# Optimization experiments

Hardware: AMD Instinct MI355X
Metric: run time of the kernel (lower is better)

The kernel has to match this reference:

```python
import jax, jax.numpy as jnp
import numpy as np

N = 4096        # batch size (rows)
K = 4           # instances per class -> num_instances in the torch code
D = 256         # embedding dim
MARGIN = 0.5
SAMPLE_KEY = jax.random.key(42)  # fixed key: deterministic stand-in for torch.multinomial


def setup_inputs() -> dict:
    key = jax.random.key(0)
    x = jax.random.normal(key, (N, D), dtype=jnp.float32)
    # L2-normalize like typical metric-learning embeddings so sims are in [-1, 1]
    inputs = x / jnp.linalg.norm(x, axis=1, keepdims=True)
    targets = (jnp.arange(N) // K).astype(jnp.int32)  # P*K batch: equal-size classes
    return {"inputs": inputs, "targets": targets}


def reference(inputs, targets):
    n = inputs.shape[0]
    km1 = K - 1                 # positives per row
    n_neg = n - K               # negatives per row

    sim = inputs @ inputs.T                                   # [n, n]
    same = targets[:, None] == targets[None, :]
    eye = jnp.eye(n, dtype=bool)
    pos_mask = same & ~eye
    neg_mask = ~same

    # masked_select + per-row sort: masked entries -> +inf, ascending sort,
    # keep first count entries (counts are uniform across rows)
    pos_sorted = jnp.sort(jnp.where(pos_mask, sim, jnp.inf), axis=1)[:, :km1]   # [n, K-1]
    neg_sorted = jnp.sort(jnp.where(neg_mask, sim, jnp.inf), axis=1)[:, :n_neg] # [n, n-K]

    pos_d = jnp.mean(pos_sorted)
    neg_d = jnp.mean(neg_sorted)

    # GaussDistribution per row over negatives
    neg_mean = jnp.mean(neg_sorted, axis=1, keepdims=True)
    neg_std = jnp.sqrt(jnp.mean((neg_sorted - neg_mean) ** 2, axis=1, keepdims=True))
    # NOTE: the original uses exp(+(x-mu)^2 / (2 sigma^2)) (no minus sign) -- faithful
    logprob = (neg_sorted - neg_mean) ** 2 / (2.0 * neg_std ** 2)               # [n, n-K]

    # multinomial without replacement ~ Gumbel top-k on log-weights
    gumbel = -jnp.log(-jnp.log(
        jax.random.uniform(SAMPLE_KEY, logprob.shape, minval=1e-20, maxval=1.0)))
    _, neg_idx = jax.lax.top_k(logprob + gumbel, km1)                            # [n, K-1]
    neg_pair = jnp.take_along_axis(neg_sorted, neg_idx, axis=1)                  # [n, K-1]

    pos_loss = jnp.mean(jnp.log1p(jnp.exp(-2.0 * (pos_sorted - MARGIN))), axis=1)
    neg_loss = 0.04 * jnp.mean(jnp.log1p(jnp.exp(50.0 * (neg_pair - MARGIN))), axis=1)
    loss = jnp.sum(pos_loss + neg_loss) / n

    # prec: fraction of rows where hardest positive > hardest sampled negative + 0.05
    c = jnp.sum(pos_sorted[:, -1] > jnp.max(neg_pair, axis=1) + 0.05)
    prec = c.astype(jnp.float32) / n

    return loss, prec, pos_d, neg_d
```

## Files before the change

kernel.cpp:

```cpp
#include <hip/hip_runtime.h>
#include <hip/hip_bf16.h>
#include <cstdint>
#include <cfloat>
#include <math.h>

#define NN 4096
#define DD 256
#define NNEG 4092
#define MARGIN 0.5f
#define NB 3584
#define NW (NB / 2)
#define GTOTAL ((uint32_t)NN * (uint32_t)NNEG)

__device__ __forceinline__ uint32_t rotl32(uint32_t x, int r) {
  return (x << r) | (x >> (32 - r));
}

__device__ __forceinline__ void threefry2x32_42(uint32_t x0, uint32_t x1,
                                                uint32_t& o0, uint32_t& o1) {
  const uint32_t k0 = 0u, k1 = 42u;
  const uint32_t k2 = k0 ^ k1 ^ 0x1BD11BDAu;
  x0 += k0; x1 += k1;
#define TF_R(r) { x0 += x1; x1 = rotl32(x1, r); x1 ^= x0; }
  TF_R(13) TF_R(15) TF_R(26) TF_R(6)
  x0 += k1; x1 += k2 + 1u;
  TF_R(17) TF_R(29) TF_R(16) TF_R(24)
  x0 += k2; x1 += k0 + 2u;
  TF_R(13) TF_R(15) TF_R(26) TF_R(6)
  x0 += k0; x1 += k1 + 3u;
  TF_R(17) TF_R(29) TF_R(16) TF_R(24)
  x0 += k1; x1 += k2 + 4u;
  TF_R(13) TF_R(15) TF_R(26) TF_R(6)
  x0 += k2; x1 += k0 + 5u;
#undef TF_R
  o0 = x0; o1 = x1;
}

__device__ __forceinline__ float gumbel_at(uint32_t f) {
  uint32_t o0, o1;
  threefry2x32_42(0u, f, o0, o1);
  uint32_t bits = o0 ^ o1;
  uint32_t fb = (bits >> 9) | 0x3F800000u;
  float fl = __uint_as_float(fb) - 1.0f;
  float u = fmaxf(1e-20f, fl + 1e-20f);
  return -logf(-logf(u));
}

__device__ __forceinline__ int bucket_of(float v) {
  return (int)fminf(fmaxf((v + 0.28f) * 6400.0f, 0.0f), (float)(NB - 1));
}

#define BT 64
#define NTT (NN / BT)
#define GEMM_BLOCKS (NTT * (NTT + 1) / 2)
#define BK 64
#define LDSS 68
#define GUMBEL_BLOCKS 384

template <int GOFF>
__global__ __launch_bounds__(256) void gemm_gumbel(const float* __restrict__ X,
                                                   float* __restrict__ S,
                                                   float* __restrict__ G) {
  __shared__ float As[BT * LDSS];
  __shared__ float Bs[BT * LDSS];
  const int tid = threadIdx.x;

  if (GOFF > 0 && (int)blockIdx.x < GOFF) {
    uint32_t i = (uint32_t)blockIdx.x * 256u + (uint32_t)tid;
    const uint32_t stride = (uint32_t)GOFF * 256u;
    for (; i < GTOTAL; i += stride) G[i] = gumbel_at(i);
    return;
  }

  const int tx = tid & 15, ty = tid >> 4;

  int b = (int)blockIdx.x - GOFF, bi = 0;
  while (b >= NTT - bi) { b -= NTT - bi; bi++; }
  const int bj = bi + b;
  const int rowBase = bi * BT, colBase = bj * BT;

  float acc[4][4] = {};
  for (int kb = 0; kb < DD; kb += BK) {
#pragma unroll
    for (int it = 0; it < 4; ++it) {
      int idx = tid + 256 * it;
      int r = idx >> 4, c4 = idx & 15;
      float4 av = *(const float4*)(X + (size_t)(rowBase + r) * DD + kb + c4 * 4);
      float4 bv = *(const float4*)(X + (size_t)(colBase + r) * DD + kb + c4 * 4);
      *(float4*)(As + r * LDSS + c4 * 4) = av;
      *(float4*)(Bs + r * LDSS + c4 * 4) = bv;
    }
    __syncthreads();
    for (int k = 0; k < BK; k += 4) {
      float4 a[4], bfr[4];
#pragma unroll
      for (int i = 0; i < 4; ++i) a[i] = *(const float4*)(As + (ty + 16 * i) * LDSS + k);
#pragma unroll
      for (int j = 0; j < 4; ++j) bfr[j] = *(const float4*)(Bs + (tx + 16 * j) * LDSS + k);
#pragma unroll
      for (int i = 0; i < 4; ++i)
#pragma unroll
        for (int j = 0; j < 4; ++j) {
          acc[i][j] += a[i].x * bfr[j].x;
          acc[i][j] += a[i].y * bfr[j].y;
          acc[i][j] += a[i].z * bfr[j].z;
          acc[i][j] += a[i].w * bfr[j].w;
        }
    }
    __syncthreads();
  }
#pragma unroll
  for (int i = 0; i < 4; ++i)
#pragma unroll
    for (int j = 0; j < 4; ++j)
      S[(size_t)(rowBase + ty + 16 * i) * NN + colBase + tx + 16 * j] = acc[i][j];
  if (bi != bj) {
#pragma unroll
    for (int i = 0; i < 4; ++i)
#pragma unroll
      for (int j = 0; j < 4; ++j)
        S[(size_t)(colBase + tx + 16 * j) * NN + rowBase + ty + 16 * i] = acc[i][j];
  }
}

#define INSERT3(sc, v)                                              \
  if ((sc) > s2) {                                                  \
    if ((sc) > s1) {                                                \
      s2 = s1; v2 = v1;                                             \
      if ((sc) > s0) { s1 = s0; v1 = v0; s0 = (sc); v0 = (v); }     \
      else           { s1 = (sc); v1 = (v); }                       \
    } else { s2 = (sc); v2 = (v); }                                 \
  }

template <int USE_G>
__global__ __launch_bounds__(256) void row_kernel(const float* __restrict__ S,
                                                  const float* __restrict__ G,
                                                  float* __restrict__ acc) {
  __shared__ uint32_t histw[NW];
  __shared__ uint32_t offsw[NW];
  __shared__ __align__(16) float sval[NN];
  __shared__ float sh[48];
  __shared__ uint32_t wtot[4];

  const int row = blockIdx.x;
  const int tid = threadIdx.x;
  const int lane = tid & 63, wid = tid >> 6;

#pragma unroll
  for (int i = 0; i < 7; ++i) histw[tid + 256 * i] = 0u;

  const float4* src = (const float4*)(S + (size_t)row * NN);
  const int pslot = row >> 2;
  float vv[16];
#pragma unroll
  for (int it = 0; it < 4; ++it) {
    int slot = tid + 256 * it;
    float4 t4 = src[slot];
    if (slot == pslot) {
      sh[16] = t4.x; sh[17] = t4.y; sh[18] = t4.z; sh[19] = t4.w;
      t4.x = INFINITY; t4.y = INFINITY; t4.z = INFINITY; t4.w = INFINITY;
    }
    vv[4 * it + 0] = t4.x; vv[4 * it + 1] = t4.y;
    vv[4 * it + 2] = t4.z; vv[4 * it + 3] = t4.w;
  }

  float s = 0.0f;
#pragma unroll
  for (int e = 0; e < 16; ++e) if (vv[e] < 1e30f) s += vv[e];
#pragma unroll
  for (int off = 32; off > 0; off >>= 1) s += __shfl_down(s, off, 64);
  if (lane == 0) sh[5 + wid] = s;
  __syncthreads();

#pragma unroll
  for (int e = 0; e < 16; ++e) {
    int b = bucket_of(vv[e]);
    atomicAdd(&histw[b >> 1], 1u << ((b & 1) << 4));
  }
  if (tid == 0) {
    int self = row & 3;
    float p[3]; int m = 0;
#pragma unroll
    for (int c = 0; c < 4; ++c)
      if (c != self) p[m++] = sh[16 + c];
    float t;
    if (p[0] > p[1]) { t = p[0]; p[0] = p[1]; p[1] = t; }
    if (p[1] > p[2]) { t = p[1]; p[1] = p[2]; p[2] = t; }
    if (p[0] > p[1]) { t = p[0]; p[0] = p[1]; p[1] = t; }
    sh[0] = p[0]; sh[1] = p[1]; sh[2] = p[2];
    float tot = sh[5] + sh[6] + sh[7] + sh[8];
    sh[9] = tot;
    sh[3] = tot / (float)NNEG;
  }
  __syncthreads();

  uint32_t hw[7];
  uint32_t s14 = 0;
#pragma unroll
  for (int j = 0; j < 7; ++j) {
    hw[j] = histw[7 * tid + j];
    s14 += (hw[j] & 0xFFFFu) + (hw[j] >> 16);
  }
  uint32_t inc = s14;
#pragma unroll
  for (int off = 1; off < 64; off <<= 1) {
    uint32_t n = __shfl_up(inc, (unsigned)off, 64);
    if (lane >= off) inc += n;
  }
  if (lane == 63) wtot[wid] = inc;

  const float mu = sh[3];
  float q = 0.0f;
#pragma unroll
  for (int e = 0; e < 16; ++e)
    if (vv[e] < 1e30f) { float d = vv[e] - mu; q += d * d; }
#pragma unroll
  for (int off = 32; off > 0; off >>= 1) q += __shfl_down(q, off, 64);
  if (lane == 0) sh[10 + wid] = q;
  __syncthreads();

  uint32_t wbase = 0;
  for (int w = 0; w < wid; ++w) wbase += wtot[w];
  uint32_t run = wbase + inc - s14;
#pragma unroll
  for (int j = 0; j < 7; ++j) {
    uint32_t lo = run; run += hw[j] & 0xFFFFu;
    uint32_t hi = run; run += hw[j] >> 16;
    offsw[7 * tid + j] = lo | (hi << 16);
  }
  if (tid == 0) {
    float var = (sh[10] + sh[11] + sh[12] + sh[13]) / (float)NNEG;
    float sd = sqrtf(var);
    sh[4] = 1.0f / (2.0f * sd * sd);
  }
  __syncthreads();

#pragma unroll
  for (int e = 0; e < 16; ++e) {
    int b = bucket_of(vv[e]);
    uint32_t old = atomicAdd(&offsw[b >> 1], 1u << ((b & 1) << 4));
    uint32_t sl = (old >> ((b & 1) << 4)) & 0xFFFFu;
    sval[sl] = vv[e];
  }
  __syncthreads();

  const float inv2s2 = sh[4];
  const uint32_t fbase = (uint32_t)row * (uint32_t)NNEG;
  const float* __restrict__ Grow = G + fbase;
  float s0 = -FLT_MAX, s1 = -FLT_MAX, s2 = -FLT_MAX;
  float v0 = 0.0f, v1 = 0.0f, v2 = 0.0f;

  float va[16]; uint32_t sten[16];
#pragma unroll
  for (int it = 0; it < 16; ++it) va[it] = sval[tid + 256 * it];
#pragma unroll
  for (int it = 0; it < 16; ++it) {
    float v = va[it];
    uint32_t pk = 0u;
    if (v < 1e30f) {
      int b = bucket_of(v);
      uint32_t sh16 = (uint32_t)((b & 1) << 4);
      uint32_t end = (offsw[b >> 1] >> sh16) & 0xFFFFu;
      uint32_t cb = (histw[b >> 1] >> sh16) & 0xFFFFu;
      pk = (end - cb) | (end << 16);
    }
    sten[it] = pk;
  }

#pragma unroll
  for (int half = 0; half < 2; ++half) {
    float4 w0[8];
#pragma unroll
    for (int j = 0; j < 8; ++j) {
      uint32_t st = sten[half * 8 + j] & 0xFFFFu;
      w0[j] = *(const float4*)(sval + (st & ~3u));
    }
#pragma unroll
    for (int j = 0; j < 8; ++j) {
      const int it = half * 8 + j;
      float v = va[it];
      if (v < 1e30f) {
        const int sl = tid + 256 * it;
        const uint32_t st = sten[it] & 0xFFFFu, en = sten[it] >> 16;
        const uint32_t nb = en - st;
        const uint32_t u0 = st & ~3u;
        int cnt = (int)st;
        {
          float4 w = w0[j];
          cnt += ((u0 + 0 - st) < nb && (w.x < v || (w.x == v && (int)(u0 + 0) < sl))) ? 1 : 0;
          cnt += ((u0 + 1 - st) < nb && (w.y < v || (w.y == v && (int)(u0 + 1) < sl))) ? 1 : 0;
          cnt += ((u0 + 2 - st) < nb && (w.z < v || (w.z == v && (int)(u0 + 2) < sl))) ? 1 : 0;
          cnt += ((u0 + 3 - st) < nb && (w.w < v || (w.w == v && (int)(u0 + 3) < sl))) ? 1 : 0;
        }
        for (uint32_t u = u0 + 4; u < en; u += 4) {
          float4 w = *(const float4*)(sval + u);
          cnt += ((u + 0 - st) < nb && (w.x < v || (w.x == v && (int)(u + 0) < sl))) ? 1 : 0;
          cnt += ((u + 1 - st) < nb && (w.y < v || (w.y == v && (int)(u + 1) < sl))) ? 1 : 0;
          cnt += ((u + 2 - st) < nb && (w.z < v || (w.z == v && (int)(u + 2) < sl))) ? 1 : 0;
          cnt += ((u + 3 - st) < nb && (w.w < v || (w.w == v && (int)(u + 3) < sl))) ? 1 : 0;
        }
        float g = USE_G ? Grow[cnt] : gumbel_at(fbase + (uint32_t)cnt);
        float d = v - mu;
        float sc = d * d * inv2s2 + g;
        INSERT3(sc, v)
      }
    }
  }

#pragma unroll
  for (int dlt = 1; dlt < 64; dlt <<= 1) {
    float t0 = __shfl_xor(s0, dlt, 64), u0 = __shfl_xor(v0, dlt, 64);
    float t1 = __shfl_xor(s1, dlt, 64), u1 = __shfl_xor(v1, dlt, 64);
    float t2 = __shfl_xor(s2, dlt, 64), u2 = __shfl_xor(v2, dlt, 64);
    INSERT3(t0, u0)
    INSERT3(t1, u1)
    INSERT3(t2, u2)
  }
  if (lane == 0) {
    int b0 = 24 + wid * 6;
    sh[b0 + 0] = s0; sh[b0 + 1] = v0;
    sh[b0 + 2] = s1; sh[b0 + 3] = v1;
    sh[b0 + 4] = s2; sh[b0 + 5] = v2;
  }
  __syncthreads();

  if (tid == 0) {
    float g0 = -FLT_MAX, g1 = -FLT_MAX, g2 = -FLT_MAX;
    float w0 = 0.0f, w1 = 0.0f, w2 = 0.0f;
    {
      float s0 = g0, s1 = g1, s2 = g2, v0 = w0, v1 = w1, v2 = w2;
#pragma unroll
      for (int i = 0; i < 12; ++i) {
        float sc = sh[24 + 2 * i], v = sh[24 + 2 * i + 1];
        INSERT3(sc, v)
      }
      g0 = s0; g1 = s1; g2 = s2; w0 = v0; w1 = v1; w2 = v2;
    }
    float negmax = fmaxf(w0, fmaxf(w1, w2));
    float neg_loss = 0.04f * (log1pf(expf(50.0f * (w0 - MARGIN))) +
                              log1pf(expf(50.0f * (w1 - MARGIN))) +
                              log1pf(expf(50.0f * (w2 - MARGIN)))) / 3.0f;
    float p0 = sh[0], p1 = sh[1], p2 = sh[2];
    float pos_loss = (log1pf(expf(-2.0f * (p0 - MARGIN))) +
                      log1pf(expf(-2.0f * (p1 - MARGIN))) +
                      log1pf(expf(-2.0f * (p2 - MARGIN)))) / 3.0f;
    atomicAdd(&acc[0], pos_loss + neg_loss);
    if (p2 > negmax + 0.05f) atomicAdd(&acc[1], 1.0f);
    atomicAdd(&acc[2], p0 + p1 + p2);
    atomicAdd(&acc[3], sh[9]);
  }
}

__global__ void finalize(const float* __restrict__ acc, float* out) {
  if (threadIdx.x == 0 && blockIdx.x == 0) {
    out[0] = acc[0] / 4096.0f;
    out[1] = acc[1] / 4096.0f;
    out[2] = acc[2] / (4096.0f * 3.0f);
    out[3] = acc[3] / (4096.0f * 4092.0f);
  }
}

extern "C" void kernel_launch(void* const* d_in, const int* in_sizes, int n_in,
                              void* d_out, int out_size, void* d_ws, size_t ws_size,
                              hipStream_t stream) {
  (void)in_sizes; (void)n_in; (void)out_size;
  const float* X = (const float*)d_in[0];
  float* S = (float*)d_ws;
  float* acc = (float*)((char*)d_ws + (size_t)NN * NN * 4);
  float* G = (float*)((char*)d_ws + (size_t)NN * NN * 4 + 256);
  const size_t need = (size_t)NN * NN * 4 + 256 + (size_t)GTOTAL * 4;
  const bool have_g = ws_size >= need;

  hipMemsetAsync(acc, 0, 4 * sizeof(float), stream);
  if (have_g) {
    gemm_gumbel<GUMBEL_BLOCKS><<<GUMBEL_BLOCKS + GEMM_BLOCKS, 256, 0, stream>>>(X, S, G);
    row_kernel<1><<<NN, 256, 0, stream>>>(S, G, acc);
  } else {
    gemm_gumbel<0><<<GEMM_BLOCKS, 256, 0, stream>>>(X, S, G);
    row_kernel<0><<<NN, 256, 0, stream>>>(S, G, acc);
  }
  finalize<<<1, 64, 0, stream>>>(acc, (float*)d_out);
}
```

Baseline: 375.0 us.

## Enlarge GEMM tiles without LDS, double row-kernel threads, widen histogram

The Gram GEMM drops LDS staging. Each thread now computes an 8x8 output block from 128x128 tiles, loading float4 operands straight from global memory and relying on cache. The per-row selection kernel moves from 256 to 512 threads with 8 elements per thread, and the histogram grows to 4096 buckets with a finer scale. The Gumbel pre-generation block count drops to 256. This trades more register pressure and uncoalesced strided global loads in the GEMM for fewer blocks, and gains more parallelism and smaller buckets in the row kernel.

```diff
diff --git a/kernel.cpp b/kernel.cpp
--- a/kernel.cpp
+++ b/kernel.cpp
@@ -8,8 +8,6 @@
 #define DD 256
 #define NNEG 4092
 #define MARGIN 0.5f
-#define NB 3584
-#define NW (NB / 2)
 #define GTOTAL ((uint32_t)NN * (uint32_t)NNEG)
 
 __device__ __forceinline__ uint32_t rotl32(uint32_t x, int r) {
@@ -46,23 +44,21 @@
   return -logf(-logf(u));
 }
 
+#define NB 4096
+#define NW (NB / 2)
 __device__ __forceinline__ int bucket_of(float v) {
-  return (int)fminf(fmaxf((v + 0.28f) * 6400.0f, 0.0f), (float)(NB - 1));
-}
-
-#define BT 64
-#define NTT (NN / BT)
-#define GEMM_BLOCKS (NTT * (NTT + 1) / 2)
-#define BK 64
-#define LDSS 68
-#define GUMBEL_BLOCKS 384
+  return (int)fminf(fmaxf((v + 0.28f) * 7314.2857f, 0.0f), (float)(NB - 1));
+}
+
+#define BT 128
+#define NT (NN / BT)
+#define GEMM_BLOCKS (NT * (NT + 1) / 2)
+#define GUMBEL_BLOCKS 256
 
 template <int GOFF>
 __global__ __launch_bounds__(256) void gemm_gumbel(const float* __restrict__ X,
                                                    float* __restrict__ S,
                                                    float* __restrict__ G) {
-  __shared__ float As[BT * LDSS];
-  __shared__ float Bs[BT * LDSS];
   const int tid = threadIdx.x;
 
   if (GOFF > 0 && (int)blockIdx.x < GOFF) {
@@ -72,53 +68,46 @@
     return;
   }
 
-  const int tx = tid & 15, ty = tid >> 4;
-
   int b = (int)blockIdx.x - GOFF, bi = 0;
-  while (b >= NTT - bi) { b -= NTT - bi; bi++; }
+  while (b >= NT - bi) { b -= NT - bi; bi++; }
   const int bj = bi + b;
   const int rowBase = bi * BT, colBase = bj * BT;
 
-  float acc[4][4] = {};
-  for (int kb = 0; kb < DD; kb += BK) {
-#pragma unroll
-    for (int it = 0; it < 4; ++it) {
-      int idx = tid + 256 * it;
-      int r = idx >> 4, c4 = idx & 15;
-      float4 av = *(const float4*)(X + (size_t)(rowBase + r) * DD + kb + c4 * 4);
-      float4 bv = *(const float4*)(X + (size_t)(colBase + r) * DD + kb + c4 * 4);
-      *(float4*)(As + r * LDSS + c4 * 4) = av;
-      *(float4*)(Bs + r * LDSS + c4 * 4) = bv;
-    }
-    __syncthreads();
-    for (int k = 0; k < BK; k += 4) {
-      float4 a[4], bfr[4];
-#pragma unroll
-      for (int i = 0; i < 4; ++i) a[i] = *(const float4*)(As + (ty + 16 * i) * LDSS + k);
-#pragma unroll
-      for (int j = 0; j < 4; ++j) bfr[j] = *(const float4*)(Bs + (tx + 16 * j) * LDSS + k);
-#pragma unroll
-      for (int i = 0; i < 4; ++i)
-#pragma unroll
-        for (int j = 0; j < 4; ++j) {
-          acc[i][j] += a[i].x * bfr[j].x;
-          acc[i][j] += a[i].y * bfr[j].y;
-          acc[i][j] += a[i].z * bfr[j].z;
-          acc[i][j] += a[i].w * bfr[j].w;
-        }
-    }
-    __syncthreads();
-  }
-#pragma unroll
-  for (int i = 0; i < 4; ++i)
-#pragma unroll
-    for (int j = 0; j < 4; ++j)
+  const int tx = tid & 15, ty = tid >> 4;
+  const float* __restrict__ pa = X + (size_t)(rowBase + ty) * DD;
+  const float* __restrict__ pb = X + (size_t)(colBase + tx) * DD;
+
+  float acc[8][8] = {};
+#pragma unroll 1
+  for (int k = 0; k < DD; k += 4) {
+    float4 a[8], bb[8];
+#pragma unroll
+    for (int i = 0; i < 8; ++i)
+      a[i] = *(const float4*)(pa + (size_t)(16 * i) * DD + k);
+#pragma unroll
+    for (int j = 0; j < 8; ++j)
+      bb[j] = *(const float4*)(pb + (size_t)(16 * j) * DD + k);
+#pragma unroll
+    for (int i = 0; i < 8; ++i)
+#pragma unroll
+      for (int j = 0; j < 8; ++j) {
+        acc[i][j] += a[i].x * bb[j].x;
+        acc[i][j] += a[i].y * bb[j].y;
+        acc[i][j] += a[i].z * bb[j].z;
+        acc[i][j] += a[i].w * bb[j].w;
+      }
+  }
+
+#pragma unroll
+  for (int i = 0; i < 8; ++i)
+#pragma unroll
+    for (int j = 0; j < 8; ++j)
       S[(size_t)(rowBase + ty + 16 * i) * NN + colBase + tx + 16 * j] = acc[i][j];
   if (bi != bj) {
 #pragma unroll
-    for (int i = 0; i < 4; ++i)
-#pragma unroll
-      for (int j = 0; j < 4; ++j)
+    for (int i = 0; i < 8; ++i)
+#pragma unroll
+      for (int j = 0; j < 8; ++j)
         S[(size_t)(colBase + tx + 16 * j) * NN + rowBase + ty + 16 * i] = acc[i][j];
   }
 }
@@ -132,29 +121,31 @@
     } else { s2 = (sc); v2 = (v); }                                 \
   }
 
+#define RE 8
+
 template <int USE_G>
-__global__ __launch_bounds__(256) void row_kernel(const float* __restrict__ S,
+__global__ __launch_bounds__(512) void row_kernel(const float* __restrict__ S,
                                                   const float* __restrict__ G,
                                                   float* __restrict__ acc) {
   __shared__ uint32_t histw[NW];
   __shared__ uint32_t offsw[NW];
   __shared__ __align__(16) float sval[NN];
-  __shared__ float sh[48];
-  __shared__ uint32_t wtot[4];
+  __shared__ float sh[128];
+  __shared__ uint32_t wtot[8];
 
   const int row = blockIdx.x;
   const int tid = threadIdx.x;
   const int lane = tid & 63, wid = tid >> 6;
 
 #pragma unroll
-  for (int i = 0; i < 7; ++i) histw[tid + 256 * i] = 0u;
+  for (int i = 0; i < 4; ++i) histw[tid + 512 * i] = 0u;
 
   const float4* src = (const float4*)(S + (size_t)row * NN);
   const int pslot = row >> 2;
-  float vv[16];
-#pragma unroll
-  for (int it = 0; it < 4; ++it) {
-    int slot = tid + 256 * it;
+  float vv[RE];
+#pragma unroll
+  for (int it = 0; it < 2; ++it) {
+    int slot = tid + 512 * it;
     float4 t4 = src[slot];
     if (slot == pslot) {
       sh[16] = t4.x; sh[17] = t4.y; sh[18] = t4.z; sh[19] = t4.w;
@@ -166,14 +157,14 @@
 
   float s = 0.0f;
 #pragma unroll
-  for (int e = 0; e < 16; ++e) if (vv[e] < 1e30f) s += vv[e];
+  for (int e = 0; e < RE; ++e) if (vv[e] < 1e30f) s += vv[e];
 #pragma unroll
   for (int off = 32; off > 0; off >>= 1) s += __shfl_down(s, off, 64);
-  if (lane == 0) sh[5 + wid] = s;
-  __syncthreads();
-
-#pragma unroll
-  for (int e = 0; e < 16; ++e) {
+  if (lane == 0) sh[32 + wid] = s;
+  __syncthreads();
+
+#pragma unroll
+  for (int e = 0; e < RE; ++e) {
     int b = bucket_of(vv[e]);
     atomicAdd(&histw[b >> 1], 1u << ((b & 1) << 4));
   }
@@ -188,20 +179,22 @@
     if (p[1] > p[2]) { t = p[1]; p[1] = p[2]; p[2] = t; }
     if (p[0] > p[1]) { t = p[0]; p[0] = p[1]; p[1] = t; }
     sh[0] = p[0]; sh[1] = p[1]; sh[2] = p[2];
-    float tot = sh[5] + sh[6] + sh[7] + sh[8];
+    float tot = 0.0f;
+#pragma unroll
+    for (int w = 0; w < 8; ++w) tot += sh[32 + w];
     sh[9] = tot;
     sh[3] = tot / (float)NNEG;
   }
   __syncthreads();
 
-  uint32_t hw[7];
-  uint32_t s14 = 0;
-#pragma unroll
-  for (int j = 0; j < 7; ++j) {
-    hw[j] = histw[7 * tid + j];
-    s14 += (hw[j] & 0xFFFFu) + (hw[j] >> 16);
-  }
-  uint32_t inc = s14;
+  uint32_t hwv[4];
+  uint32_t s8 = 0;
+#pragma unroll
+  for (int j = 0; j < 4; ++j) {
+    hwv[j] = histw[4 * tid + j];
+    s8 += (hwv[j] & 0xFFFFu) + (hwv[j] >> 16);
+  }
+  uint32_t inc = s8;
 #pragma unroll
   for (int off = 1; off < 64; off <<= 1) {
     uint32_t n = __shfl_up(inc, (unsigned)off, 64);
@@ -212,31 +205,34 @@
   const float mu = sh[3];
   float q = 0.0f;
 #pragma unroll
-  for (int e = 0; e < 16; ++e)
+  for (int e = 0; e < RE; ++e)
     if (vv[e] < 1e30f) { float d = vv[e] - mu; q += d * d; }
 #pragma unroll
   for (int off = 32; off > 0; off >>= 1) q += __shfl_down(q, off, 64);
-  if (lane == 0) sh[10 + wid] = q;
+  if (lane == 0) sh[48 + wid] = q;
   __syncthreads();
 
   uint32_t wbase = 0;
   for (int w = 0; w < wid; ++w) wbase += wtot[w];
-  uint32_t run = wbase + inc - s14;
-#pragma unroll
-  for (int j = 0; j < 7; ++j) {
-    uint32_t lo = run; run += hw[j] & 0xFFFFu;
-    uint32_t hi = run; run += hw[j] >> 16;
-    offsw[7 * tid + j] = lo | (hi << 16);
+  uint32_t run = wbase + inc - s8;
+#pragma unroll
+  for (int j = 0; j < 4; ++j) {
+    uint32_t lo = run; run += hwv[j] & 0xFFFFu;
+    uint32_t hi = run; run += hwv[j] >> 16;
+    offsw[4 * tid + j] = lo | (hi << 16);
   }
   if (tid == 0) {
-    float var = (sh[10] + sh[11] + sh[12] + sh[13]) / (float)NNEG;
+    float var = 0.0f;
+#pragma unroll
+    for (int w = 0; w < 8; ++w) var += sh[48 + w];
+    var /= (float)NNEG;
     float sd = sqrtf(var);
     sh[4] = 1.0f / (2.0f * sd * sd);
   }
   __syncthreads();
 
 #pragma unroll
-  for (int e = 0; e < 16; ++e) {
+  for (int e = 0; e < RE; ++e) {
     int b = bucket_of(vv[e]);
     uint32_t old = atomicAdd(&offsw[b >> 1], 1u << ((b & 1) << 4));
     uint32_t sl = (old >> ((b & 1) << 4)) & 0xFFFFu;
@@ -250,11 +246,11 @@
   float s0 = -FLT_MAX, s1 = -FLT_MAX, s2 = -FLT_MAX;
   float v0 = 0.0f, v1 = 0.0f, v2 = 0.0f;
 
-  float va[16]; uint32_t sten[16];
-#pragma unroll
-  for (int it = 0; it < 16; ++it) va[it] = sval[tid + 256 * it];
-#pragma unroll
-  for (int it = 0; it < 16; ++it) {
+  float va[RE]; uint32_t sten[RE];
+#pragma unroll
+  for (int it = 0; it < RE; ++it) va[it] = sval[tid + 512 * it];
+#pragma unroll
+  for (int it = 0; it < RE; ++it) {
     float v = va[it];
     uint32_t pk = 0u;
     if (v < 1e30f) {
@@ -267,43 +263,39 @@
     sten[it] = pk;
   }
 
-#pragma unroll
-  for (int half = 0; half < 2; ++half) {
-    float4 w0[8];
-#pragma unroll
-    for (int j = 0; j < 8; ++j) {
-      uint32_t st = sten[half * 8 + j] & 0xFFFFu;
-      w0[j] = *(const float4*)(sval + (st & ~3u));
-    }
-#pragma unroll
-    for (int j = 0; j < 8; ++j) {
-      const int it = half * 8 + j;
-      float v = va[it];
-      if (v < 1e30f) {
-        const int sl = tid + 256 * it;
-        const uint32_t st = sten[it] & 0xFFFFu, en = sten[it] >> 16;
-        const uint32_t nb = en - st;
-        const uint32_t u0 = st & ~3u;
-        int cnt = (int)st;
-        {
-          float4 w = w0[j];
-          cnt += ((u0 + 0 - st) < nb && (w.x < v || (w.x == v && (int)(u0 + 0) < sl))) ? 1 : 0;
-          cnt += ((u0 + 1 - st) < nb && (w.y < v || (w.y == v && (int)(u0 + 1) < sl))) ? 1 : 0;
-          cnt += ((u0 + 2 - st) < nb && (w.z < v || (w.z == v && (int)(u0 + 2) < sl))) ? 1 : 0;
-          cnt += ((u0 + 3 - st) < nb && (w.w < v || (w.w == v && (int)(u0 + 3) < sl))) ? 1 : 0;
-        }
-        for (uint32_t u = u0 + 4; u < en; u += 4) {
-          float4 w = *(const float4*)(sval + u);
-          cnt += ((u + 0 - st) < nb && (w.x < v || (w.x == v && (int)(u + 0) < sl))) ? 1 : 0;
-          cnt += ((u + 1 - st) < nb && (w.y < v || (w.y == v && (int)(u + 1) < sl))) ? 1 : 0;
-          cnt += ((u + 2 - st) < nb && (w.z < v || (w.z == v && (int)(u + 2) < sl))) ? 1 : 0;
-          cnt += ((u + 3 - st) < nb && (w.w < v || (w.w == v && (int)(u + 3) < sl))) ? 1 : 0;
-        }
-        float g = USE_G ? Grow[cnt] : gumbel_at(fbase + (uint32_t)cnt);
-        float d = v - mu;
-        float sc = d * d * inv2s2 + g;
-        INSERT3(sc, v)
+  float4 w0[RE];
+#pragma unroll
+  for (int j = 0; j < RE; ++j) {
+    uint32_t st = sten[j] & 0xFFFFu;
+    w0[j] = *(const float4*)(sval + (st & ~3u));
+  }
+#pragma unroll
+  for (int j = 0; j < RE; ++j) {
+    float v = va[j];
+    if (v < 1e30f) {
+      const int sl = tid + 512 * j;
+      const uint32_t st = sten[j] & 0xFFFFu, en = sten[j] >> 16;
+      const uint32_t nb = en - st;
+      const uint32_t u0 = st & ~3u;
+      int cnt = (int)st;
+      {
+        float4 w = w0[j];
+        cnt += ((u0 + 0 - st) < nb && (w.x < v || (w.x == v && (int)(u0 + 0) < sl))) ? 1 : 0;
+        cnt += ((u0 + 1 - st) < nb && (w.y < v || (w.y == v && (int)(u0 + 1) < sl))) ? 1 : 0;
+        cnt += ((u0 + 2 - st) < nb && (w.z < v || (w.z == v && (int)(u0 + 2) < sl))) ? 1 : 0;
+        cnt += ((u0 + 3 - st) < nb && (w.w < v || (w.w == v && (int)(u0 + 3) < sl))) ? 1 : 0;
       }
+      for (uint32_t u = u0 + 4; u < en; u += 4) {
+        float4 w = *(const float4*)(sval + u);
+        cnt += ((u + 0 - st) < nb && (w.x < v || (w.x == v && (int)(u + 0) < sl))) ? 1 : 0;
+        cnt += ((u + 1 - st) < nb && (w.y < v || (w.y == v && (int)(u + 1) < sl))) ? 1 : 0;
+        cnt += ((u + 2 - st) < nb && (w.z < v || (w.z == v && (int)(u + 2) < sl))) ? 1 : 0;
+        cnt += ((u + 3 - st) < nb && (w.w < v || (w.w == v && (int)(u + 3) < sl))) ? 1 : 0;
+      }
+      float g = USE_G ? Grow[cnt] : gumbel_at(fbase + (uint32_t)cnt);
+      float d = v - mu;
+      float sc = d * d * inv2s2 + g;
+      INSERT3(sc, v)
     }
   }
 
@@ -317,7 +309,7 @@
     INSERT3(t2, u2)
   }
   if (lane == 0) {
-    int b0 = 24 + wid * 6;
+    int b0 = 64 + wid * 6;
     sh[b0 + 0] = s0; sh[b0 + 1] = v0;
     sh[b0 + 2] = s1; sh[b0 + 3] = v1;
     sh[b0 + 4] = s2; sh[b0 + 5] = v2;
@@ -326,20 +318,19 @@
 
   if (tid == 0) {
     float g0 = -FLT_MAX, g1 = -FLT_MAX, g2 = -FLT_MAX;
-    float w0 = 0.0f, w1 = 0.0f, w2 = 0.0f;
+    float w0s = 0.0f, w1s = 0.0f, w2s = 0.0f;
     {
-      float s0 = g0, s1 = g1, s2 = g2, v0 = w0, v1 = w1, v2 = w2;
-#pragma unroll
-      for (int i = 0; i < 12; ++i) {
-        float sc = sh[24 + 2 * i], v = sh[24 + 2 * i + 1];
+      float s0 = g0, s1 = g1, s2 = g2, v0 = w0s, v1 = w1s, v2 = w2s;
+      for (int i = 0; i < 24; ++i) {
+        float sc = sh[64 + 2 * i], v = sh[64 + 2 * i + 1];
         INSERT3(sc, v)
       }
-      g0 = s0; g1 = s1; g2 = s2; w0 = v0; w1 = v1; w2 = v2;
+      g0 = s0; g1 = s1; g2 = s2; w0s = v0; w1s = v1; w2s = v2;
     }
-    float negmax = fmaxf(w0, fmaxf(w1, w2));
-    float neg_loss = 0.04f * (log1pf(expf(50.0f * (w0 - MARGIN))) +
-                              log1pf(expf(50.0f * (w1 - MARGIN))) +
-                              log1pf(expf(50.0f * (w2 - MARGIN)))) / 3.0f;
+    float negmax = fmaxf(w0s, fmaxf(w1s, w2s));
+    float neg_loss = 0.04f * (log1pf(expf(50.0f * (w0s - MARGIN))) +
+                              log1pf(expf(50.0f * (w1s - MARGIN))) +
+                              log1pf(expf(50.0f * (w2s - MARGIN)))) / 3.0f;
     float p0 = sh[0], p1 = sh[1], p2 = sh[2];
     float pos_loss = (log1pf(expf(-2.0f * (p0 - MARGIN))) +
                       log1pf(expf(-2.0f * (p1 - MARGIN))) +
@@ -374,10 +365,10 @@
   hipMemsetAsync(acc, 0, 4 * sizeof(float), stream);
   if (have_g) {
     gemm_gumbel<GUMBEL_BLOCKS><<<GUMBEL_BLOCKS + GEMM_BLOCKS, 256, 0, stream>>>(X, S, G);
-    row_kernel<1><<<NN, 256, 0, stream>>>(S, G, acc);
+    row_kernel<1><<<NN, 512, 0, stream>>>(S, G, acc);
   } else {
     gemm_gumbel<0><<<GEMM_BLOCKS, 256, 0, stream>>>(X, S, G);
-    row_kernel<0><<<NN, 256, 0, stream>>>(S, G, acc);
+    row_kernel<0><<<NN, 512, 0, stream>>>(S, G, acc);
   }
   finalize<<<1, 64, 0, stream>>>(acc, (float*)d_out);
 }
```

Result: slower. 523.6 us (+39.6%).
